# Kernel tuning notes

Measured on AMD Instinct MI355X. Metric: run time of the kernel, lower is better.

## Reference

```python
import jax, jax.numpy as jnp
import numpy as np

H, D_IN, D_ATT, D_OUT, S, T = 16, 1024, 64, 64, 2048, 2048


def setup_inputs() -> dict:
    key = jax.random.key(0)
    ks = jax.random.split(key, 12)
    s = lambda fan_in: 1.0 / np.sqrt(fan_in)
    inp = {
        "current_tokens": jax.random.normal(ks[0], (S, D_IN), jnp.float32),
        "context_tokens": jax.random.normal(ks[1], (T, D_IN), jnp.float32),
        # per-head projection weights (stacked over heads)
        "Wq": jax.random.uniform(ks[2], (H, D_IN, D_ATT), jnp.float32, -s(D_IN), s(D_IN)),
        "bq": jax.random.uniform(ks[3], (H, D_ATT), jnp.float32, -s(D_IN), s(D_IN)),
        "Wk": jax.random.uniform(ks[4], (H, D_IN, D_ATT), jnp.float32, -s(D_IN), s(D_IN)),
        "bk": jax.random.uniform(ks[5], (H, D_ATT), jnp.float32, -s(D_IN), s(D_IN)),
        "Wv": jax.random.uniform(ks[6], (H, D_IN, D_OUT), jnp.float32, -s(D_IN), s(D_IN)),
        "bv": jax.random.uniform(ks[7], (H, D_OUT), jnp.float32, -s(D_IN), s(D_IN)),
        # out_proj: Linear(H*D_OUT -> D_OUT)
        "Wo": jax.random.uniform(ks[8], (H * D_OUT, D_OUT), jnp.float32, -s(H * D_OUT), s(H * D_OUT)),
        "bo": jax.random.uniform(ks[9], (D_OUT,), jnp.float32, -s(H * D_OUT), s(H * D_OUT)),
    }
    return inp


def reference(current_tokens, context_tokens, Wq, bq, Wk, bk, Wv, bv, Wo, bo):
    # Batched over heads: q,k: [H,S/T,D_ATT], v: [H,T,D_OUT]
    q = jnp.einsum("si,hid->hsd", current_tokens, Wq) + bq[:, None, :]
    k = jnp.einsum("ti,hid->htd", context_tokens, Wk) + bk[:, None, :]
    v = jnp.einsum("ti,hio->hto", context_tokens, Wv) + bv[:, None, :]
    scores = jnp.einsum("hsd,htd->hst", q, k) / jnp.sqrt(jnp.asarray(D_ATT, q.dtype))
    attn = jax.nn.softmax(scores, axis=-1)          # [H,S,T]
    y = jnp.einsum("hst,hto->hso", attn, v)          # [H,S,D_OUT]
    # torch.cat(ys, dim=0) -> [H*S, D_OUT]; .view(-1, H*D_OUT) -> [S, H*D_OUT]
    # (row-major reshape of head-major stacking, exactly as the torch code does)
    y = y.reshape(-1, D_OUT).reshape(-1, H * D_OUT)
    return y @ Wo + bo                               # [S, D_OUT]
```

## Files before the change

### kernel.cpp

```cpp
#include <hip/hip_runtime.h>

#define DEV static __device__ __forceinline__

typedef unsigned short u16;
typedef unsigned int u32;
typedef float f32x4 __attribute__((ext_vector_type(4)));
typedef __bf16 bf16x8 __attribute__((ext_vector_type(8)));
typedef unsigned short u16x8 __attribute__((ext_vector_type(8)));
typedef unsigned int u32x2 __attribute__((ext_vector_type(2)));
typedef unsigned int u32x4 __attribute__((ext_vector_type(4)));

constexpr int H = 16, DIN = 1024, DH = 64, S = 2048, T = 2048;
constexpr float SM_C = 0.18033688011112042f;

DEV u16 f2bf(float f) { return __builtin_bit_cast(u16, (__bf16)f); }
DEV float bf2f(u16 u) { u32 i = (u32)u << 16; return __builtin_bit_cast(float, i); }
DEV bf16x8 ld_bf8(const u16* p) { return __builtin_bit_cast(bf16x8, *(const u16x8*)p); }
DEV u32 cvtpk(float lo, float hi) {
  u32 r; asm("v_cvt_pk_bf16_f32 %0, %1, %2" : "=v"(r) : "v"(lo), "v"(hi)); return r;
}

#define GLOAD16(gp, lp) __builtin_amdgcn_global_load_lds( \
    (const __attribute__((address_space(1))) void*)(gp),  \
    (__attribute__((address_space(3))) void*)(lp), 16, 0, 0)

__global__ __launch_bounds__(256) void prep_kernel(
    const float* __restrict__ cur, const float* __restrict__ ctx,
    const float* __restrict__ Wq, const float* __restrict__ Wk,
    const float* __restrict__ Wv, const float* __restrict__ Wo,
    u16* __restrict__ cur_bf, u16* __restrict__ ctx_bf,
    u16* __restrict__ WqT, u16* __restrict__ WkvT, u16* __restrict__ WoT) {
  __shared__ alignas(16) float tile[64 * 68];
  int bid = blockIdx.x, tid = threadIdx.x;
  if (bid < 2048) {
    int i = bid * 256 + tid;
    const float* in; u16* out; int j;
    if (i < 262144) { in = cur; out = cur_bf; j = i; }
    else            { in = ctx; out = ctx_bf; j = i - 262144; }
    const float4* p = (const float4*)(in + (size_t)j * 8);
    float4 x = p[0], y = p[1];
    u16x8 o;
    o[0] = f2bf(x.x); o[1] = f2bf(x.y); o[2] = f2bf(x.z); o[3] = f2bf(x.w);
    o[4] = f2bf(y.x); o[5] = f2bf(y.y); o[6] = f2bf(y.z); o[7] = f2bf(y.w);
    *(u16x8*)(out + (size_t)j * 8) = o;
    return;
  }
  int t = bid - 2048, k0 = (t & 15) * 64, y = t >> 4;
  const float* W; u16* Wt; float scale = 1.0f;
  if (y < 16)      { W = Wq + (size_t)y * DIN * DH;        Wt = WqT + (size_t)y * DH * DIN; scale = SM_C; }
  else if (y < 32) { W = Wk + (size_t)(y - 16) * DIN * DH; Wt = WkvT + (size_t)(y - 16) * DH * DIN; }
  else if (y < 48) { W = Wv + (size_t)(y - 32) * DIN * DH; Wt = WkvT + (size_t)(y - 16) * DH * DIN; }
  else             { W = Wo;                               Wt = WoT; }
#pragma unroll
  for (int it = 0; it < 4; ++it) {
    int slot = it * 256 + tid;
    int i = slot >> 4, j4 = (slot & 15) * 4;
    *(float4*)&tile[i * 68 + j4] = *(const float4*)&W[(size_t)(k0 + i) * 64 + j4];
  }
  __syncthreads();
  int n = tid >> 2, kb = (tid & 3) * 16;
  u16x8 o0, o1;
#pragma unroll
  for (int j = 0; j < 8; ++j) o0[j] = f2bf(tile[(kb + j) * 68 + n] * scale);
#pragma unroll
  for (int j = 0; j < 8; ++j) o1[j] = f2bf(tile[(kb + 8 + j) * 68 + n] * scale);
  *(u16x8*)&Wt[(size_t)n * DIN + k0 + kb] = o0;
  *(u16x8*)&Wt[(size_t)n * DIN + k0 + kb + 8] = o1;
}

__global__ __launch_bounds__(256) void gemm_qkv_kernel(
    const u16* __restrict__ Acur, const u16* __restrict__ Actx,
    const u16* __restrict__ WqT, const u16* __restrict__ WkvT,
    const float* __restrict__ bq, const float* __restrict__ bk, const float* __restrict__ bv,
    u16* __restrict__ Qall, u16* __restrict__ Kall, u16* __restrict__ VtAll) {
  __shared__ alignas(16) u16 As[2][128 * 64];
  __shared__ alignas(16) u16 Bs[2][64 * 64];
  int bid = blockIdx.x;
  const u16 *A, *W; int m0, n0, mode;
  if (bid < 256)      { A = Acur; W = WqT;               m0 = (bid >> 4) * 128;  n0 = (bid & 15) * 64; mode = 0; }
  else if (bid < 512) { int b = bid - 256; A = Actx; W = WkvT;               m0 = (b >> 4) * 128; n0 = (b & 15) * 64; mode = 1; }
  else                { int b = bid - 512; A = Actx; W = WkvT + 1024 * 1024; m0 = (b >> 4) * 128; n0 = (b & 15) * 64; mode = 2; }
  int tid = threadIdx.x, w = tid >> 6, l = tid & 63, g = l >> 4, r = l & 15;
  auto stage = [&](int buf, int kt) {
#pragma unroll
    for (int it = 0; it < 4; ++it) {
      int c = it * 256 + tid, row = c >> 3, q = c & 7;
      GLOAD16(&A[(size_t)(m0 + row) * DIN + kt + ((q ^ (row & 7)) << 3)], &As[buf][c * 8]);
    }
#pragma unroll
    for (int it = 0; it < 2; ++it) {
      int c = it * 256 + tid, row = c >> 3, q = c & 7;
      GLOAD16(&W[(size_t)(n0 + row) * DIN + kt + ((q ^ (row & 7)) << 3)], &Bs[buf][c * 8]);
    }
  };
  stage(0, 0);
  __syncthreads();
  f32x4 acc[2][4] = {};
  for (int t = 0; t < 16; ++t) {
    if (t < 15) stage((t + 1) & 1, (t + 1) * 64);
    int cur = t & 1;
#pragma unroll
    for (int kk = 0; kk < 2; ++kk) {
      int qo = (((kk << 2) | g) ^ (r & 7)) << 3;
      bf16x8 a0 = ld_bf8(&As[cur][(w * 32 + r) * 64 + qo]);
      bf16x8 a1 = ld_bf8(&As[cur][(w * 32 + 16 + r) * 64 + qo]);
      if (mode < 2) {
#pragma unroll
        for (int nf = 0; nf < 4; ++nf) {
          bf16x8 b = ld_bf8(&Bs[cur][(nf * 16 + r) * 64 + qo]);
          acc[0][nf] = __builtin_amdgcn_mfma_f32_16x16x32_bf16(a0, b, acc[0][nf], 0, 0, 0);
          acc[1][nf] = __builtin_amdgcn_mfma_f32_16x16x32_bf16(a1, b, acc[1][nf], 0, 0, 0);
        }
      } else {
#pragma unroll
        for (int nf = 0; nf < 4; ++nf) {
          bf16x8 b = ld_bf8(&Bs[cur][(nf * 16 + r) * 64 + qo]);
          acc[0][nf] = __builtin_amdgcn_mfma_f32_16x16x32_bf16(b, a0, acc[0][nf], 0, 0, 0);
          acc[1][nf] = __builtin_amdgcn_mfma_f32_16x16x32_bf16(b, a1, acc[1][nf], 0, 0, 0);
        }
      }
    }
    __syncthreads();
  }
  if (mode < 2) {
    u16* dst = (mode == 0) ? Qall : Kall;
    const float* bias = (mode == 0) ? bq : bk;
    float bscale = (mode == 0) ? SM_C : 1.0f;
#pragma unroll
    for (int mi = 0; mi < 2; ++mi)
#pragma unroll
      for (int nf = 0; nf < 4; ++nf)
#pragma unroll
        for (int rr = 0; rr < 4; ++rr) {
          int row = m0 + w * 32 + mi * 16 + 4 * g + rr, col = n0 + nf * 16 + r;
          dst[(size_t)row * 1024 + col] = f2bf(acc[mi][nf][rr] + bias[col] * bscale);
        }
  } else {
#pragma unroll
    for (int mi = 0; mi < 2; ++mi)
#pragma unroll
      for (int nf = 0; nf < 4; ++nf)
#pragma unroll
        for (int rr = 0; rr < 4; ++rr) {
          int d = n0 + nf * 16 + 4 * g + rr, tok = m0 + w * 32 + mi * 16 + r;
          VtAll[(size_t)d * 2048 + tok] = f2bf(acc[mi][nf][rr] + bv[d]);
        }
  }
}

__global__ __launch_bounds__(256, 2) void attn_kernel(
    const u16* __restrict__ Qall, const u16* __restrict__ Kall,
    const u16* __restrict__ VtAll, u16* __restrict__ OP, float* __restrict__ LP) {
  int qb = blockIdx.x, h = blockIdx.y, ts = blockIdx.z;
  int tid = threadIdx.x, w = tid >> 6, l = tid & 63, g = l >> 4, r = l & 15;
  __shared__ alignas(16) u16 Ks[2][64 * 64];
  __shared__ alignas(16) u16 Vs[2][64 * 64];
  const int q0 = qb * 256 + w * 64;
  bf16x8 qf[4][2];
#pragma unroll
  for (int sub = 0; sub < 4; ++sub)
#pragma unroll
    for (int kk = 0; kk < 2; ++kk)
      qf[sub][kk] = ld_bf8(&Qall[(size_t)(q0 + sub * 16 + r) * 1024 + h * 64 + kk * 32 + 8 * g]);
  f32x4 o[4][4] = {};
  float lsum[4] = {0.f, 0.f, 0.f, 0.f};
  const int tBeg = ts * 512, tEnd = tBeg + 512;

  auto stage = [&](int buf, int t0) {
#pragma unroll
    for (int it = 0; it < 2; ++it) {
      int c = it * 256 + tid, row = c >> 3, q = c & 7;
      int qs = (q ^ (row & 7)) << 3;
      GLOAD16(&Kall[(size_t)(t0 + row) * 1024 + h * 64 + qs], &Ks[buf][c * 8]);
      GLOAD16(&VtAll[(size_t)(h * 64 + row) * 2048 + t0 + qs], &Vs[buf][c * 8]);
    }
  };
  stage(0, tBeg);
  __syncthreads();
  int cur = 0;
  for (int t0 = tBeg; t0 < tEnd; t0 += 64) {
    if (t0 + 64 < tEnd) stage(cur ^ 1, t0 + 64);
    f32x4 sacc[4][4] = {};
#pragma unroll
    for (int kk = 0; kk < 2; ++kk) {
      int qo = (((kk << 2) | g) ^ (r & 7)) << 3;
#pragma unroll
      for (int nf = 0; nf < 4; ++nf) {
        bf16x8 kf = ld_bf8(&Ks[cur][(nf * 16 + r) * 64 + qo]);
#pragma unroll
        for (int sub = 0; sub < 4; ++sub)
          sacc[sub][nf] = __builtin_amdgcn_mfma_f32_16x16x32_bf16(kf, qf[sub][kk], sacc[sub][nf], 0, 0, 0);
      }
    }
    u32 c[4][4][2];
#pragma unroll
    for (int sub = 0; sub < 4; ++sub)
#pragma unroll
      for (int nf = 0; nf < 4; ++nf) {
        float p0 = __builtin_amdgcn_exp2f(sacc[sub][nf][0]);
        float p1 = __builtin_amdgcn_exp2f(sacc[sub][nf][1]);
        float p2 = __builtin_amdgcn_exp2f(sacc[sub][nf][2]);
        float p3 = __builtin_amdgcn_exp2f(sacc[sub][nf][3]);
        lsum[sub] += (p0 + p1) + (p2 + p3);
        c[sub][nf][0] = cvtpk(p0, p1);
        c[sub][nf][1] = cvtpk(p2, p3);
      }
#pragma unroll
    for (int kk = 0; kk < 2; ++kk) {
      int qo = (((kk << 2) | g) ^ (r & 7)) << 3;
      bf16x8 vf[4];
#pragma unroll
      for (int nf = 0; nf < 4; ++nf) vf[nf] = ld_bf8(&Vs[cur][(nf * 16 + r) * 64 + qo]);
#pragma unroll
      for (int sub = 0; sub < 4; ++sub) {
        u32 dw[4];
#pragma unroll
        for (int s2 = 0; s2 < 2; ++s2) {
          u32x2 t1 = __builtin_amdgcn_permlane32_swap(c[sub][2 * kk][s2], c[sub][2 * kk + 1][s2],
                                                      false, false);
          u32x2 t2 = __builtin_amdgcn_permlane16_swap(t1.x, t1.y, false, false);
          dw[s2] = t2.x; dw[2 + s2] = t2.y;
        }
        bf16x8 pB = __builtin_bit_cast(bf16x8, (u32x4){dw[0], dw[1], dw[2], dw[3]});
#pragma unroll
        for (int nf = 0; nf < 4; ++nf)
          o[sub][nf] = __builtin_amdgcn_mfma_f32_16x16x32_bf16(vf[nf], pB, o[sub][nf], 0, 0, 0);
      }
    }
    __syncthreads();
    cur ^= 1;
  }
#pragma unroll
  for (int sub = 0; sub < 4; ++sub) {
    float ls = lsum[sub];
    ls += __shfl_xor(ls, 16, 64);
    ls += __shfl_xor(ls, 32, 64);
    int s = q0 + sub * 16 + r;
    if (l < 16) LP[(size_t)(ts * 16 + h) * 2048 + s] = ls;
#pragma unroll
    for (int nf = 0; nf < 4; ++nf) {
      uint2 pd;
      pd.x = cvtpk(o[sub][nf][0], o[sub][nf][1]);
      pd.y = cvtpk(o[sub][nf][2], o[sub][nf][3]);
      *(uint2*)&OP[((size_t)(ts * 16 + h) * 2048 + s) * 64 + nf * 16 + 4 * g] = pd;
    }
  }
}

__global__ __launch_bounds__(256) void oproj_part_kernel(const u16* __restrict__ OP,
                                                         const float* __restrict__ LP,
                                                         const u16* __restrict__ WoT,
                                                         float* __restrict__ Part) {
  __shared__ alignas(16) u16 As[128 * 64];
  __shared__ alignas(16) u16 Bs[64 * 64];
  int bx = blockIdx.x, kz = blockIdx.y, kt = kz * 64;
  int tid = threadIdx.x, w = tid >> 6, l = tid & 63, g = l >> 4, r = l & 15;
#pragma unroll
  for (int it = 0; it < 2; ++it) {
    int c = it * 256 + tid, row = c >> 3, q = c & 7;
    GLOAD16(&WoT[(size_t)row * DIN + kt + ((q ^ (row & 7)) << 3)], &Bs[c * 8]);
  }
#pragma unroll
  for (int it = 0; it < 4; ++it) {
    int c = it * 256 + tid, row = c >> 3, q = c & 7, qs = q ^ (row & 7);
    int s = row * 16 + kz;
    float a8[8] = {};
    float lsum = 0.f;
#pragma unroll
    for (int ts = 0; ts < 4; ++ts) {
      u16x8 v = *(const u16x8*)&OP[((size_t)(ts * 16 + bx) * 2048 + s) * 64 + qs * 8];
#pragma unroll
      for (int e = 0; e < 8; ++e) a8[e] += bf2f(v[e]);
      lsum += LP[(size_t)(ts * 16 + bx) * 2048 + s];
    }
    float inv = 1.0f / lsum;
    u16x8 ov;
#pragma unroll
    for (int e = 0; e < 8; ++e) ov[e] = f2bf(a8[e] * inv);
    *(u16x8*)&As[c * 8] = ov;
  }
  __syncthreads();
  f32x4 acc[2][4] = {};
#pragma unroll
  for (int kk = 0; kk < 2; ++kk) {
    int qo = (((kk << 2) | g) ^ (r & 7)) << 3;
    bf16x8 a0 = ld_bf8(&As[(w * 32 + r) * 64 + qo]);
    bf16x8 a1 = ld_bf8(&As[(w * 32 + 16 + r) * 64 + qo]);
#pragma unroll
    for (int nf = 0; nf < 4; ++nf) {
      bf16x8 b = ld_bf8(&Bs[(nf * 16 + r) * 64 + qo]);
      acc[0][nf] = __builtin_amdgcn_mfma_f32_16x16x32_bf16(a0, b, acc[0][nf], 0, 0, 0);
      acc[1][nf] = __builtin_amdgcn_mfma_f32_16x16x32_bf16(a1, b, acc[1][nf], 0, 0, 0);
    }
  }
#pragma unroll
  for (int mi = 0; mi < 2; ++mi)
#pragma unroll
    for (int nf = 0; nf < 4; ++nf)
#pragma unroll
      for (int rr = 0; rr < 4; ++rr)
        Part[((size_t)kz * 2048 + bx * 128 + w * 32 + mi * 16 + 4 * g + rr) * 64 + nf * 16 + r] =
            acc[mi][nf][rr];
}

__global__ __launch_bounds__(256) void oproj_reduce_kernel(const float* __restrict__ Part,
                                                           const float* __restrict__ bo,
                                                           float* __restrict__ out) {
  int i = blockIdx.x * 256 + threadIdx.x;
  float s = bo[i & 63];
#pragma unroll
  for (int kz = 0; kz < 16; ++kz) s += Part[(size_t)kz * 131072 + i];
  out[i] = s;
}

extern "C" void kernel_launch(void* const* d_in, const int* in_sizes, int n_in,
                              void* d_out, int out_size, void* d_ws, size_t ws_size,
                              hipStream_t stream) {
  const float* cur = (const float*)d_in[0];
  const float* ctx = (const float*)d_in[1];
  const float* Wq = (const float*)d_in[2];
  const float* bq = (const float*)d_in[3];
  const float* Wk = (const float*)d_in[4];
  const float* bk = (const float*)d_in[5];
  const float* Wv = (const float*)d_in[6];
  const float* bv = (const float*)d_in[7];
  const float* Wo = (const float*)d_in[8];
  const float* bo = (const float*)d_in[9];
  float* out = (float*)d_out;

  char* ws = (char*)d_ws;
  const size_t MB = 1ull << 20;
  u16* cur_bf = (u16*)(ws + 0 * MB);
  u16* ctx_bf = (u16*)(ws + 4 * MB);
  u16* WqT    = (u16*)(ws + 8 * MB);
  u16* WkvT   = (u16*)(ws + 10 * MB);
  u16* WoT    = (u16*)(ws + 14 * MB);
  u16* Qall   = (u16*)(ws + 15 * MB);
  u16* Kall   = (u16*)(ws + 19 * MB);
  u16* VtAll  = (u16*)(ws + 23 * MB);
  u16* OP     = (u16*)(ws + 27 * MB);
  float* LP   = (float*)(ws + 43 * MB);
  float* Part = (float*)(ws + 44 * MB);

  prep_kernel<<<2832, 256, 0, stream>>>(cur, ctx, Wq, Wk, Wv, Wo, cur_bf, ctx_bf,
                                        WqT, WkvT, WoT);
  gemm_qkv_kernel<<<768, 256, 0, stream>>>(cur_bf, ctx_bf, WqT, WkvT, bq, bk, bv,
                                           Qall, Kall, VtAll);
  attn_kernel<<<dim3(8, 16, 4), 256, 0, stream>>>(Qall, Kall, VtAll, OP, LP);
  oproj_part_kernel<<<dim3(16, 16), 256, 0, stream>>>(OP, LP, WoT, Part);
  oproj_reduce_kernel<<<512, 256, 0, stream>>>(Part, bo, out);
}
```

Before: 68.69 us.

## Quad-buffer K/V tiles in attention, add MFMA priority hints, vectorize reduce

The attention kernel now uses four LDS buffers, staging two 64-token tiles ahead and computing two tiles per barrier. This halves the number of __syncthreads and deepens prefetch. s_setprio is raised around the MFMA sections so matrix work is favoured over the exp phase of other waves. The o-proj reduce kernel now loads and stores float4, using a quarter of the blocks. LDS use doubles to 64KB per block, which may limit occupancy at 2 blocks per CU.

```diff
diff --git a/kernel.cpp b/kernel.cpp
--- a/kernel.cpp
+++ b/kernel.cpp
@@ -153,8 +153,8 @@
     const u16* __restrict__ VtAll, u16* __restrict__ OP, float* __restrict__ LP) {
   int qb = blockIdx.x, h = blockIdx.y, ts = blockIdx.z;
   int tid = threadIdx.x, w = tid >> 6, l = tid & 63, g = l >> 4, r = l & 15;
-  __shared__ alignas(16) u16 Ks[2][64 * 64];
-  __shared__ alignas(16) u16 Vs[2][64 * 64];
+  __shared__ alignas(16) u16 Ks[4][64 * 64];
+  __shared__ alignas(16) u16 Vs[4][64 * 64];
   const int q0 = qb * 256 + w * 64;
   bf16x8 qf[4][2];
 #pragma unroll
@@ -164,7 +164,7 @@
       qf[sub][kk] = ld_bf8(&Qall[(size_t)(q0 + sub * 16 + r) * 1024 + h * 64 + kk * 32 + 8 * g]);
   f32x4 o[4][4] = {};
   float lsum[4] = {0.f, 0.f, 0.f, 0.f};
-  const int tBeg = ts * 512, tEnd = tBeg + 512;
+  const int tBeg = ts * 512;
 
   auto stage = [&](int buf, int t0) {
 #pragma unroll
@@ -175,23 +175,21 @@
       GLOAD16(&VtAll[(size_t)(h * 64 + row) * 2048 + t0 + qs], &Vs[buf][c * 8]);
     }
   };
-  stage(0, tBeg);
-  __syncthreads();
-  int cur = 0;
-  for (int t0 = tBeg; t0 < tEnd; t0 += 64) {
-    if (t0 + 64 < tEnd) stage(cur ^ 1, t0 + 64);
+  auto compute = [&](int buf) {
     f32x4 sacc[4][4] = {};
+    __builtin_amdgcn_s_setprio(1);
 #pragma unroll
     for (int kk = 0; kk < 2; ++kk) {
       int qo = (((kk << 2) | g) ^ (r & 7)) << 3;
 #pragma unroll
       for (int nf = 0; nf < 4; ++nf) {
-        bf16x8 kf = ld_bf8(&Ks[cur][(nf * 16 + r) * 64 + qo]);
+        bf16x8 kf = ld_bf8(&Ks[buf][(nf * 16 + r) * 64 + qo]);
 #pragma unroll
         for (int sub = 0; sub < 4; ++sub)
           sacc[sub][nf] = __builtin_amdgcn_mfma_f32_16x16x32_bf16(kf, qf[sub][kk], sacc[sub][nf], 0, 0, 0);
       }
     }
+    __builtin_amdgcn_s_setprio(0);
     u32 c[4][4][2];
 #pragma unroll
     for (int sub = 0; sub < 4; ++sub)
@@ -205,12 +203,13 @@
         c[sub][nf][0] = cvtpk(p0, p1);
         c[sub][nf][1] = cvtpk(p2, p3);
       }
+    __builtin_amdgcn_s_setprio(1);
 #pragma unroll
     for (int kk = 0; kk < 2; ++kk) {
       int qo = (((kk << 2) | g) ^ (r & 7)) << 3;
       bf16x8 vf[4];
 #pragma unroll
-      for (int nf = 0; nf < 4; ++nf) vf[nf] = ld_bf8(&Vs[cur][(nf * 16 + r) * 64 + qo]);
+      for (int nf = 0; nf < 4; ++nf) vf[nf] = ld_bf8(&Vs[buf][(nf * 16 + r) * 64 + qo]);
 #pragma unroll
       for (int sub = 0; sub < 4; ++sub) {
         u32 dw[4];
@@ -227,8 +226,20 @@
           o[sub][nf] = __builtin_amdgcn_mfma_f32_16x16x32_bf16(vf[nf], pB, o[sub][nf], 0, 0, 0);
       }
     }
+    __builtin_amdgcn_s_setprio(0);
+  };
+
+  stage(0, tBeg);
+  stage(1, tBeg + 64);
+  __syncthreads();
+  for (int tt = 0; tt < 8; tt += 2) {
+    if (tt + 2 < 8) {
+      stage((tt + 2) & 3, tBeg + (tt + 2) * 64);
+      stage((tt + 3) & 3, tBeg + (tt + 3) * 64);
+    }
+    compute(tt & 3);
+    compute((tt + 1) & 3);
     __syncthreads();
-    cur ^= 1;
   }
 #pragma unroll
   for (int sub = 0; sub < 4; ++sub) {
@@ -306,11 +317,15 @@
 __global__ __launch_bounds__(256) void oproj_reduce_kernel(const float* __restrict__ Part,
                                                            const float* __restrict__ bo,
                                                            float* __restrict__ out) {
-  int i = blockIdx.x * 256 + threadIdx.x;
-  float s = bo[i & 63];
-#pragma unroll
-  for (int kz = 0; kz < 16; ++kz) s += Part[(size_t)kz * 131072 + i];
-  out[i] = s;
+  int i4 = (blockIdx.x * 256 + threadIdx.x) * 4;
+  int d = i4 & 63;
+  float4 s = {bo[d], bo[d + 1], bo[d + 2], bo[d + 3]};
+#pragma unroll
+  for (int kz = 0; kz < 16; ++kz) {
+    float4 p = *(const float4*)&Part[(size_t)kz * 131072 + i4];
+    s.x += p.x; s.y += p.y; s.z += p.z; s.w += p.w;
+  }
+  *(float4*)&out[i4] = s;
 }
 
 extern "C" void kernel_launch(void* const* d_in, const int* in_sizes, int n_in,
@@ -348,5 +363,5 @@
                                            Qall, Kall, VtAll);
   attn_kernel<<<dim3(8, 16, 4), 256, 0, stream>>>(Qall, Kall, VtAll, OP, LP);
   oproj_part_kernel<<<dim3(16, 16), 256, 0, stream>>>(OP, LP, WoT, Part);
-  oproj_reduce_kernel<<<512, 256, 0, stream>>>(Part, bo, out);
-}
+  oproj_reduce_kernel<<<128, 256, 0, stream>>>(Part, bo, out);
+}
```

Result: slower. 70.81 us (+3.1%).
